# Performance work log

Hardware: AMD Instinct MI355X
Metric: run time of the kernel (lower is better)

The kernel has to match this reference:

```python
import jax, jax.numpy as jnp
import numpy as np

N_NODES = 20000
N_EDGES = 320000
IN_DIM = 128
HID = 256
HEADS = 8
DH = HID // HEADS  # 32
LAYERS = 3
NUM_GRAPHS = 64
OUT_DIM = 10
SLOPE = 0.2  # DGL GATv2Conv default negative_slope


def setup_inputs() -> dict:
    key = jax.random.key(0)
    ks = jax.random.split(key, 20)
    s_in = 1.0 / np.sqrt(IN_DIM)
    s_h = 1.0 / np.sqrt(HID)
    s_h2 = 1.0 / np.sqrt(HID // 2)
    return {
        "feature": jax.random.normal(ks[0], (N_NODES, IN_DIM), jnp.float32),
        "W_in": jax.random.normal(ks[1], (IN_DIM, HID), jnp.float32) * s_in,
        "b_in": jax.random.normal(ks[2], (HID,), jnp.float32) * 0.01,
        "W_src": jax.random.normal(ks[3], (LAYERS, HID, HID), jnp.float32) * s_h,
        "b_src": jax.random.normal(ks[4], (LAYERS, HID), jnp.float32) * 0.01,
        "W_dst": jax.random.normal(ks[5], (LAYERS, HID, HID), jnp.float32) * s_h,
        "b_dst": jax.random.normal(ks[6], (LAYERS, HID), jnp.float32) * 0.01,
        "attn": jax.random.normal(ks[7], (LAYERS, HEADS, DH), jnp.float32) * (1.0 / np.sqrt(DH)),
        "Wc1": jax.random.normal(ks[8], (HID, HID), jnp.float32) * s_h,
        "bc1": jax.random.normal(ks[9], (HID,), jnp.float32) * 0.01,
        "Wc2": jax.random.normal(ks[10], (HID, HID // 2), jnp.float32) * s_h,
        "bc2": jax.random.normal(ks[11], (HID // 2,), jnp.float32) * 0.01,
        "Wc3": jax.random.normal(ks[12], (HID // 2, OUT_DIM), jnp.float32) * s_h2,
        "bc3": jax.random.normal(ks[13], (OUT_DIM,), jnp.float32) * 0.01,
        "src": jax.random.randint(ks[14], (N_EDGES,), 0, N_NODES, jnp.int32),
        "dst": jax.random.randint(ks[15], (N_EDGES,), 0, N_NODES, jnp.int32),
        "graph_ids": jnp.sort(jax.random.randint(ks[16], (N_NODES,), 0, NUM_GRAPHS, jnp.int32)),
    }


def _gatv2_layer(h, Ws, bs, Wd, bd, a, src, dst):
    # DGL GATv2Conv: e_ij = a^T LeakyReLU(W_src h_j + W_dst h_i), edge softmax over
    # incoming edges of dst, scatter-sum of alpha * W_src h_src; residual = Identity
    # (in_feats == heads*out_feats); activation relu.
    n = h.shape[0]
    fs = (h @ Ws + bs).reshape(n, HEADS, DH)  # [N,H,D]
    fd = (h @ Wd + bd).reshape(n, HEADS, DH)
    e = jax.nn.leaky_relu(fs[src] + fd[dst], SLOPE)          # [E,H,D]
    score = jnp.einsum("ehd,hd->eh", e, a)                   # [E,H]
    m = jax.ops.segment_max(score, dst, num_segments=n)       # stable softmax max
    ex = jnp.exp(score - m[dst])
    denom = jax.ops.segment_sum(ex, dst, num_segments=n)
    alpha = ex / denom[dst]                                    # [E,H]
    rst = jax.ops.segment_sum(alpha[:, :, None] * fs[src], dst, num_segments=n)
    out = jax.nn.relu(rst + h.reshape(n, HEADS, DH))          # residual + activation
    return out.reshape(n, HID)


def reference(feature, W_in, b_in, W_src, b_src, W_dst, b_dst, attn,
              Wc1, bc1, Wc2, bc2, Wc3, bc3, src, dst, graph_ids):
    h = feature @ W_in + b_in
    for l in range(LAYERS):
        h = _gatv2_layer(h, W_src[l], b_src[l], W_dst[l], b_dst[l], attn[l], src, dst)
    # dgl.sum_nodes over batched graph -> per-graph segment sum
    hg = jax.ops.segment_sum(h, graph_ids, num_segments=NUM_GRAPHS)  # [G,HID]
    # classifier (dropout is identity in eval mode)
    x = jax.nn.relu(hg @ Wc1 + bc1)
    x = jax.nn.relu(x @ Wc2 + bc2)
    return x @ Wc3 + bc3  # [G,OUT_DIM]
```

## Files before the change

### kernel.cpp

```cpp
#include <hip/hip_runtime.h>
#include <hip/hip_bf16.h>
#include <math.h>

#define N_NODES 20000
#define N_EDGES 320000
#define IN_DIM 128
#define HID 256
#define HEADS 8
#define DH 32
#define LAYERS 3
#define NUM_GRAPHS 64
#define OUT_DIM 10
#define SLOPE 0.2f

#define NBKT 5
#define N_BINS (N_NODES * NBKT)
#define SCAN_BLK 1024
#define SCAN_NBLK ((N_BINS + SCAN_BLK - 1) / SCAN_BLK)

typedef __bf16 bf16x8 __attribute__((ext_vector_type(8)));
typedef float f32x4 __attribute__((ext_vector_type(4)));

static __device__ __forceinline__ unsigned short f2bfbits(float v) {
    __bf16 b = (__bf16)v;
    return __builtin_bit_cast(unsigned short, b);
}
static __device__ __forceinline__ void unpack8(uint4 u, float* f) {
    unsigned p0 = u.x, p1 = u.y, p2 = u.z, p3 = u.w;
    f[0] = __builtin_bit_cast(float, p0 << 16);
    f[1] = __builtin_bit_cast(float, p0 & 0xffff0000u);
    f[2] = __builtin_bit_cast(float, p1 << 16);
    f[3] = __builtin_bit_cast(float, p1 & 0xffff0000u);
    f[4] = __builtin_bit_cast(float, p2 << 16);
    f[5] = __builtin_bit_cast(float, p2 & 0xffff0000u);
    f[6] = __builtin_bit_cast(float, p3 << 16);
    f[7] = __builtin_bit_cast(float, p3 & 0xffff0000u);
}
static __device__ __forceinline__ void unpack4(uint2 u, float* f) {
    f[0] = __builtin_bit_cast(float, u.x << 16);
    f[1] = __builtin_bit_cast(float, u.x & 0xffff0000u);
    f[2] = __builtin_bit_cast(float, u.y << 16);
    f[3] = __builtin_bit_cast(float, u.y & 0xffff0000u);
}

typedef const __attribute__((address_space(1))) unsigned int* as1_u32p;
typedef __attribute__((address_space(3))) unsigned int* as3_u32p;
static __device__ __forceinline__ void async_cp16(const unsigned short* g, unsigned short* l) {
    __builtin_amdgcn_global_load_lds((as1_u32p)g, (as3_u32p)l, 16, 0, 0);
}

#define CAST_N4 (N_NODES * IN_DIM / 4)
#define WTRANS_TOTAL (IN_DIM * HID + 6 * HID * HID)
#define ZERO_TOTAL (N_BINS + NUM_GRAPHS * HID)
#define PREP_TOTAL (CAST_N4 + WTRANS_TOTAL + ZERO_TOTAL)
__global__ void prep_kernel(const float* __restrict__ feat,
                            const float* __restrict__ Win,
                            const float* __restrict__ Wsrc,
                            const float* __restrict__ Wdst,
                            unsigned short* __restrict__ featH,
                            unsigned short* __restrict__ WinT,
                            unsigned short* __restrict__ WT,
                            int* __restrict__ cnt, float* __restrict__ hg) {
    int idx = blockIdx.x * blockDim.x + threadIdx.x;
    if (idx < CAST_N4) {
        float4 v = ((const float4*)feat)[idx];
        ushort4 o;
        o.x = f2bfbits(v.x); o.y = f2bfbits(v.y);
        o.z = f2bfbits(v.z); o.w = f2bfbits(v.w);
        ((ushort4*)featH)[idx] = o;
    } else if (idx < CAST_N4 + WTRANS_TOTAL) {
        int j = idx - CAST_N4;
        if (j < IN_DIM * HID) {
            int n = j / IN_DIM, k = j % IN_DIM;
            WinT[j] = f2bfbits(Win[k * HID + n]);
        } else {
            int r6 = j - IN_DIM * HID;
            int mat = r6 >> 16;
            int r = r6 & 65535;
            int n = r >> 8, k = r & 255;
            const float* base = (mat < 3) ? (Wsrc + (size_t)mat * 65536)
                                          : (Wdst + (size_t)(mat - 3) * 65536);
            WT[r6] = f2bfbits(base[k * 256 + n]);
        }
    } else if (idx < PREP_TOTAL) {
        int z = idx - CAST_N4 - WTRANS_TOTAL;
        if (z < N_BINS) cnt[z] = 0;
        else hg[z - N_BINS] = 0.f;
    }
}

__global__ void count_kernel(const int* __restrict__ src, const int* __restrict__ dst,
                             int* __restrict__ cnt) {
    int e = blockIdx.x * blockDim.x + threadIdx.x;
    if (e < N_EDGES) atomicAdd(&cnt[dst[e] * NBKT + (src[e] >> 12)], 1);
}

__global__ __launch_bounds__(1024) void scan_partial(const int* __restrict__ cnt,
                                                     int* __restrict__ bsum) {
    __shared__ int wsum[16];
    int t = threadIdx.x;
    int idx = blockIdx.x * SCAN_BLK + t;
    int x = (idx < N_BINS) ? cnt[idx] : 0;
    int v = x;
#pragma unroll
    for (int d = 1; d < 64; d <<= 1) v += __shfl_xor(v, d, 64);
    if ((t & 63) == 0) wsum[t >> 6] = v;
    __syncthreads();
    if (t == 0) {
        int s = 0;
#pragma unroll
        for (int i = 0; i < 16; ++i) s += wsum[i];
        bsum[blockIdx.x] = s;
    }
}

__global__ __launch_bounds__(1024) void scan_scatter(const int* __restrict__ cnt,
                                                     const int* __restrict__ bsum,
                                                     int* __restrict__ offs,
                                                     int* __restrict__ cursor) {
    __shared__ int wsum[16];
    __shared__ int bpart[128];
    __shared__ int sbase;
    int t = threadIdx.x;
    int blk = blockIdx.x;
    if (t < 128) bpart[t] = (t < blk) ? bsum[t] : 0;
    __syncthreads();
    if (t < 64) {
        int r = bpart[t] + bpart[t + 64];
#pragma unroll
        for (int d = 1; d < 64; d <<= 1) r += __shfl_xor(r, d, 64);
        if (t == 0) sbase = r;
    }
    int idx = blk * SCAN_BLK + t;
    int x = (idx < N_BINS) ? cnt[idx] : 0;
    int v = x;
#pragma unroll
    for (int d = 1; d < 64; d <<= 1) {
        int u = __shfl_up(v, d, 64);
        if ((t & 63) >= d) v += u;
    }
    if ((t & 63) == 63) wsum[t >> 6] = v;
    __syncthreads();
    if (t < 16) {
        int wv = wsum[t];
#pragma unroll
        for (int d = 1; d < 16; d <<= 1) {
            int u = __shfl_up(wv, d, 64);
            if (t >= d) wv += u;
        }
        wsum[t] = wv;
    }
    __syncthreads();
    int waveoff = (t >> 6) ? wsum[(t >> 6) - 1] : 0;
    int ex = sbase + waveoff + v - x;
    if (idx < N_BINS) { offs[idx] = ex; cursor[idx] = ex; }
    if (blk == SCAN_NBLK - 1 && t == SCAN_BLK - 1) offs[N_BINS] = ex + x;
}

__global__ void fill_kernel(const int* __restrict__ src, const int* __restrict__ dst,
                            int* __restrict__ cursor, int* __restrict__ csr_src) {
    int e = blockIdx.x * blockDim.x + threadIdx.x;
    if (e < N_EDGES) {
        int sv = src[e];
        int p = atomicAdd(&cursor[dst[e] * NBKT + (sv >> 12)], 1);
        csr_src[p] = sv;
    }
}

template <int DUAL>
__global__ __launch_bounds__(256, 4) void mfma_gemm(
    const unsigned short* __restrict__ Ah,
    const unsigned short* __restrict__ BT1, const float* __restrict__ bias1,
    unsigned short* __restrict__ O1,
    const unsigned short* __restrict__ BT2, const float* __restrict__ bias2,
    unsigned short* __restrict__ O2,
    int M, int K, int N) {
    __shared__ __align__(16) unsigned short As[2][64 * 32];
    __shared__ __align__(16) unsigned short Bs1[2][128 * 32];
    __shared__ __align__(16) unsigned short Bs2[DUAL ? 2 : 1][DUAL ? 128 * 32 : 8];

    const int t = threadIdx.x;
    const int wv = t >> 6, lane = t & 63, quad = lane >> 4, l15 = lane & 15;
    const int m0 = blockIdx.x * 64, n0 = blockIdx.y * 128;

    const int sA = wv * 64 + lane;
    const int rA = sA >> 2, cA = (sA & 3) ^ ((rA >> 1) & 3);
    int gmA = m0 + rA; if (gmA >= M) gmA = M - 1;
    const size_t offA = (size_t)gmA * K + cA * 8;
    const int sB0 = wv * 64 + lane, sB1v = sB0 + 256;
    const int rB0 = sB0 >> 2, cB0 = (sB0 & 3) ^ ((rB0 >> 1) & 3);
    const int rB1 = sB1v >> 2, cB1 = (sB1v & 3) ^ ((rB1 >> 1) & 3);
    const size_t offB0 = (size_t)(n0 + rB0) * K + cB0 * 8;
    const size_t offB1 = (size_t)(n0 + rB1) * K + cB1 * 8;

    auto issue = [&](int buf, int k0) {
        async_cp16(Ah + offA + k0, &As[buf][wv * 512]);
        async_cp16(BT1 + offB0 + k0, &Bs1[buf][wv * 512]);
        async_cp16(BT1 + offB1 + k0, &Bs1[buf][2048 + wv * 512]);
        if (DUAL) {
            async_cp16(BT2 + offB0 + k0, &Bs2[buf][wv * 512]);
            async_cp16(BT2 + offB1 + k0, &Bs2[buf][2048 + wv * 512]);
        }
    };

    const int mrow0 = (wv >> 1) * 32;
    const int ncb = (wv & 1) * 64;

    f32x4 zero = {0.f, 0.f, 0.f, 0.f};
    f32x4 acc1[2][4], acc2[2][4];
#pragma unroll
    for (int mi = 0; mi < 2; ++mi)
#pragma unroll
        for (int t4 = 0; t4 < 4; ++t4) { acc1[mi][t4] = zero; acc2[mi][t4] = zero; }

    issue(0, 0);
    int buf = 0;
    for (int k0 = 0; k0 < K; k0 += 32, buf ^= 1) {
        __syncthreads();
        if (k0 + 32 < K) issue(buf ^ 1, k0 + 32);

        bf16x8 aF[2];
#pragma unroll
        for (int mi = 0; mi < 2; ++mi) {
            int row = mrow0 + mi * 16 + l15;
            int aoff = row * 32 + ((quad ^ ((row >> 1) & 3)) << 3);
            aF[mi] = __builtin_bit_cast(bf16x8, *(const uint4*)(&As[buf][0] + aoff));
        }
#pragma unroll
        for (int t4 = 0; t4 < 4; ++t4) {
            int brow = ncb + t4 * 16 + l15;
            int boff = brow * 32 + ((quad ^ ((brow >> 1) & 3)) << 3);
            bf16x8 b1 = __builtin_bit_cast(bf16x8, *(const uint4*)(&Bs1[buf][0] + boff));
#pragma unroll
            for (int mi = 0; mi < 2; ++mi)
                acc1[mi][t4] = __builtin_amdgcn_mfma_f32_16x16x32_bf16(aF[mi], b1, acc1[mi][t4], 0, 0, 0);
            if (DUAL) {
                bf16x8 b2 = __builtin_bit_cast(bf16x8, *(const uint4*)(&Bs2[buf][0] + boff));
#pragma unroll
                for (int mi = 0; mi < 2; ++mi)
                    acc2[mi][t4] = __builtin_amdgcn_mfma_f32_16x16x32_bf16(aF[mi], b2, acc2[mi][t4], 0, 0, 0);
            }
        }
    }

    float bia1[4], bia2[4];
#pragma unroll
    for (int t4 = 0; t4 < 4; ++t4) {
        bia1[t4] = bias1[n0 + ncb + t4 * 16 + l15];
        bia2[t4] = DUAL ? bias2[n0 + ncb + t4 * 16 + l15] : 0.f;
    }
#pragma unroll
    for (int mi = 0; mi < 2; ++mi) {
#pragma unroll
        for (int t4 = 0; t4 < 4; ++t4) {
            int gn = n0 + ncb + t4 * 16 + l15;
#pragma unroll
            for (int r = 0; r < 4; ++r) {
                int gm = m0 + mrow0 + mi * 16 + quad * 4 + r;
                if (gm < M) {
                    float v = acc1[mi][t4][r] + bia1[t4];
                    O1[(size_t)gm * N + gn] = f2bfbits(v);
                    if (DUAL) {
                        float v2 = acc2[mi][t4][r] + bia2[t4];
                        O2[(size_t)gm * N + gn] = f2bfbits(v2);
                    }
                }
            }
        }
    }
}

__global__ __launch_bounds__(256) void gat_agg2(
    const unsigned short* __restrict__ fsb, const unsigned short* __restrict__ fdb,
    unsigned short* __restrict__ hb, const int* __restrict__ offs,
    const int* __restrict__ csr_src, const float* __restrict__ attn_l) {
    int tid = threadIdx.x;
    int node = (blockIdx.x * blockDim.x + tid) >> 5;
    if (node >= N_NODES) return;
    int l32 = tid & 31;
    int dbase = l32 * 8;
    int abase = (l32 >> 2) * DH + (l32 & 3) * 8;

    float a[8];
#pragma unroll
    for (int j = 0; j < 8; ++j) a[j] = attn_l[abase + j];

    float fdv[8];
    unpack8(*(const uint4*)(fdb + (size_t)node * HID + dbase), fdv);

    float ssum0 = 0.f, ssum1 = 0.f;
    float acc0[8], acc1[8];
#pragma unroll
    for (int j = 0; j < 8; ++j) { acc0[j] = 0.f; acc1[j] = 0.f; }

    auto procE = [&](uint4 u, float* acc, float& ssum) {
        float fsv[8];
        unpack8(u, fsv);
        float p = 0.f;
#pragma unroll
        for (int j = 0; j < 8; ++j) {
            float e = fsv[j] + fdv[j];
            e = fmaxf(e, SLOPE * e);
            p += e * a[j];
        }
        p += __shfl_xor(p, 1, 64);
        p += __shfl_xor(p, 2, 64);
        float w = __expf(p);
        ssum += w;
#pragma unroll
        for (int j = 0; j < 8; ++j) acc[j] += w * fsv[j];
    };

    const unsigned short* fsl = fsb + dbase;
    int beg = offs[node * NBKT], end = offs[node * NBKT + NBKT];
    int nfull = (end - beg) >> 2;
    const int limit = beg + nfull * 4;

    uint4 cu0, cu1, cu2, cu3;
    int ci0, ci1, ci2, ci3;
    int base = beg + 8;
    bool have = (nfull >= 1);
    bool haveN = (nfull >= 2);
    if (have) {
        int s0 = csr_src[beg], s1 = csr_src[beg + 1];
        int s2 = csr_src[beg + 2], s3 = csr_src[beg + 3];
        if (haveN) {
            ci0 = csr_src[beg + 4]; ci1 = csr_src[beg + 5];
            ci2 = csr_src[beg + 6]; ci3 = csr_src[beg + 7];
        }
        cu0 = *(const uint4*)(fsl + (size_t)s0 * HID);
        cu1 = *(const uint4*)(fsl + (size_t)s1 * HID);
        cu2 = *(const uint4*)(fsl + (size_t)s2 * HID);
        cu3 = *(const uint4*)(fsl + (size_t)s3 * HID);
    }
    while (have) {
        uint4 nu0, nu1, nu2, nu3;
        int ni0, ni1, ni2, ni3;
        if (haveN) {
            nu0 = *(const uint4*)(fsl + (size_t)ci0 * HID);
            nu1 = *(const uint4*)(fsl + (size_t)ci1 * HID);
            nu2 = *(const uint4*)(fsl + (size_t)ci2 * HID);
            nu3 = *(const uint4*)(fsl + (size_t)ci3 * HID);
        }
        bool haveNN = (base + 4 <= limit);
        if (haveNN) {
            ni0 = csr_src[base]; ni1 = csr_src[base + 1];
            ni2 = csr_src[base + 2]; ni3 = csr_src[base + 3];
        }
        base += 4;
        procE(cu0, acc0, ssum0);
        procE(cu1, acc1, ssum1);
        procE(cu2, acc0, ssum0);
        procE(cu3, acc1, ssum1);
        if (haveN) { cu0 = nu0; cu1 = nu1; cu2 = nu2; cu3 = nu3; }
        if (haveNN) { ci0 = ni0; ci1 = ni1; ci2 = ni2; ci3 = ni3; }
        have = haveN; haveN = haveNN;
    }
    for (int idx = limit; idx < end; ++idx) {
        int sv = csr_src[idx];
        procE(*(const uint4*)(fsl + (size_t)sv * HID), acc0, ssum0);
    }

    float ssum = ssum0 + ssum1;
    float acc[8];
#pragma unroll
    for (int j = 0; j < 8; ++j) acc[j] = acc0[j] + acc1[j];

    float inv = ssum > 0.f ? 1.f / ssum : 0.f;
    float hv[8];
    unpack8(*(const uint4*)(hb + (size_t)node * HID + dbase), hv);
    unsigned short ob[8];
#pragma unroll
    for (int j = 0; j < 8; ++j) {
        float o = fmaxf(acc[j] * inv + hv[j], 0.f);
        ob[j] = f2bfbits(o);
    }
    *(uint4*)(hb + (size_t)node * HID + dbase) = *(uint4*)ob;
}

#define POOL_CHUNK 32
__global__ __launch_bounds__(64) void pool_kernel(const unsigned short* __restrict__ hb,
                                                  const int* __restrict__ gid,
                                                  float* __restrict__ hg) {
    int t = threadIdx.x;
    int n0 = blockIdx.x * POOL_CHUNK;
    int n1 = n0 + POOL_CHUNK; if (n1 > N_NODES) n1 = N_NODES;
    if (n0 >= N_NODES) return;
    float acc[4] = {0.f, 0.f, 0.f, 0.f};
    int cur = gid[n0];
    for (int n = n0; n < n1; ++n) {
        int g = gid[n];
        if (g != cur) {
            atomicAdd(&hg[(size_t)cur * HID + t * 4 + 0], acc[0]);
            atomicAdd(&hg[(size_t)cur * HID + t * 4 + 1], acc[1]);
            atomicAdd(&hg[(size_t)cur * HID + t * 4 + 2], acc[2]);
            atomicAdd(&hg[(size_t)cur * HID + t * 4 + 3], acc[3]);
            acc[0] = acc[1] = acc[2] = acc[3] = 0.f;
            cur = g;
        }
        float v[4];
        unpack4(*(const uint2*)(hb + (size_t)n * HID + t * 4), v);
        acc[0] += v[0]; acc[1] += v[1]; acc[2] += v[2]; acc[3] += v[3];
    }
    atomicAdd(&hg[(size_t)cur * HID + t * 4 + 0], acc[0]);
    atomicAdd(&hg[(size_t)cur * HID + t * 4 + 1], acc[1]);
    atomicAdd(&hg[(size_t)cur * HID + t * 4 + 2], acc[2]);
    atomicAdd(&hg[(size_t)cur * HID + t * 4 + 3], acc[3]);
}

__global__ __launch_bounds__(256) void classifier_kernel(
    const float* __restrict__ hg,
    const float* __restrict__ Wc1, const float* __restrict__ bc1,
    const float* __restrict__ Wc2, const float* __restrict__ bc2,
    const float* __restrict__ Wc3, const float* __restrict__ bc3,
    float* __restrict__ out) {
    __shared__ float xin[HID];
    __shared__ float x1[HID];
    __shared__ float x2[HID / 2];
    int g = blockIdx.x, t = threadIdx.x;
    xin[t] = hg[(size_t)g * HID + t];
    __syncthreads();
    {
        float acc = bc1[t];
        for (int k = 0; k < HID; ++k) acc += xin[k] * Wc1[k * HID + t];
        x1[t] = fmaxf(acc, 0.f);
    }
    __syncthreads();
    if (t < HID / 2) {
        float acc = bc2[t];
        for (int k = 0; k < HID; ++k) acc += x1[k] * Wc2[k * (HID / 2) + t];
        x2[t] = fmaxf(acc, 0.f);
    }
    __syncthreads();
    if (t < OUT_DIM) {
        float acc = bc3[t];
        for (int k = 0; k < HID / 2; ++k) acc += x2[k] * Wc3[k * OUT_DIM + t];
        out[g * OUT_DIM + t] = acc;
    }
}

extern "C" void kernel_launch(void* const* d_in, const int* in_sizes, int n_in,
                              void* d_out, int out_size, void* d_ws, size_t ws_size,
                              hipStream_t stream) {
    const float* feature = (const float*)d_in[0];
    const float* W_in   = (const float*)d_in[1];
    const float* b_in   = (const float*)d_in[2];
    const float* W_src  = (const float*)d_in[3];
    const float* b_src  = (const float*)d_in[4];
    const float* W_dst  = (const float*)d_in[5];
    const float* b_dst  = (const float*)d_in[6];
    const float* attn   = (const float*)d_in[7];
    const float* Wc1    = (const float*)d_in[8];
    const float* bc1    = (const float*)d_in[9];
    const float* Wc2    = (const float*)d_in[10];
    const float* bc2    = (const float*)d_in[11];
    const float* Wc3    = (const float*)d_in[12];
    const float* bc3    = (const float*)d_in[13];
    const int* src     = (const int*)d_in[14];
    const int* dst     = (const int*)d_in[15];
    const int* gid     = (const int*)d_in[16];
    float* out = (float*)d_out;

    char* w = (char*)d_ws;
    auto alloc = [&](size_t bytes) -> void* {
        void* p = (void*)w;
        w += (bytes + 255) & ~(size_t)255;
        return p;
    };
    unsigned short* hb  = (unsigned short*)alloc((size_t)N_NODES * HID * 2);
    unsigned short* fsb = (unsigned short*)alloc((size_t)N_NODES * HID * 2);
    unsigned short* fdb = (unsigned short*)alloc((size_t)N_NODES * HID * 2);
    float* hg    = (float*)alloc((size_t)NUM_GRAPHS * HID * 4);
    int* cnt     = (int*)alloc((size_t)N_BINS * 4);
    int* offs    = (int*)alloc((size_t)(N_BINS + 1) * 4);
    int* cursor  = (int*)alloc((size_t)N_BINS * 4);
    int* csr_src = (int*)alloc((size_t)N_EDGES * 4);
    int* bsum    = (int*)alloc((size_t)SCAN_NBLK * 4);
    unsigned short* WinT = (unsigned short*)alloc((size_t)IN_DIM * HID * 2);
    unsigned short* WT   = (unsigned short*)alloc((size_t)6 * HID * HID * 2);
    unsigned short* featH = (unsigned short*)alloc((size_t)N_NODES * IN_DIM * 2);
    (void)alloc(4096);

    hipLaunchKernelGGL(prep_kernel, dim3((PREP_TOTAL + 255) / 256), dim3(256), 0, stream,
                       feature, W_in, W_src, W_dst, featH, WinT, WT, cnt, hg);

    hipLaunchKernelGGL(count_kernel, dim3((N_EDGES + 255) / 256), dim3(256), 0, stream,
                       src, dst, cnt);
    hipLaunchKernelGGL(scan_partial, dim3(SCAN_NBLK), dim3(SCAN_BLK), 0, stream, cnt, bsum);
    hipLaunchKernelGGL(scan_scatter, dim3(SCAN_NBLK), dim3(SCAN_BLK), 0, stream,
                       cnt, bsum, offs, cursor);
    hipLaunchKernelGGL(fill_kernel, dim3((N_EDGES + 255) / 256), dim3(256), 0, stream,
                       src, dst, cursor, csr_src);

    dim3 ggrid((N_NODES + 63) / 64, HID / 128);

    hipLaunchKernelGGL((mfma_gemm<0>), ggrid, dim3(256), 0, stream,
                       featH, WinT, b_in, hb,
                       (const unsigned short*)nullptr, (const float*)nullptr,
                       (unsigned short*)nullptr,
                       N_NODES, IN_DIM, HID);

    for (int l = 0; l < LAYERS; ++l) {
        hipLaunchKernelGGL((mfma_gemm<1>), ggrid, dim3(256), 0, stream,
                           hb,
                           WT + (size_t)l * HID * HID, b_src + (size_t)l * HID, fsb,
                           WT + (size_t)(3 + l) * HID * HID, b_dst + (size_t)l * HID, fdb,
                           N_NODES, HID, HID);
        hipLaunchKernelGGL(gat_agg2, dim3(N_NODES / 8), dim3(256), 0, stream,
                           fsb, fdb, hb, offs, csr_src, attn + (size_t)l * HEADS * DH);
    }

    hipLaunchKernelGGL(pool_kernel, dim3((N_NODES + POOL_CHUNK - 1) / POOL_CHUNK), dim3(64), 0, stream,
                       hb, gid, hg);
    hipLaunchKernelGGL(classifier_kernel, dim3(NUM_GRAPHS), dim3(256), 0, stream,
                       hg, Wc1, bc1, Wc2, bc2, Wc3, bc3, out);
}
```

Baseline: 313.7 us.

## Fuse preprocessing, CSR build, and pooling into co-scheduled combined kernels

Edge counting now shares a launch with the weight and feature casts. A single-block vectorised scan runs alongside the input GEMM tiles, and the CSR fill runs alongside the first layer's dual GEMM. Graph pooling moves into the classifier kernel: each block binary-searches the sorted graph ids and sums its node range directly, replacing the atomic pool kernel and the zeroing of its buffer. The aim is fewer kernel launches and less serialization, at the cost of a long sequential single-block scan and uneven blocks within the fused grids.

New measurement: 388.2 us. 1.24x slower.

```diff
diff --git a/kernel.cpp b/kernel.cpp
--- a/kernel.cpp
+++ b/kernel.cpp
@@ -15,8 +15,11 @@
 
 #define NBKT 5
 #define N_BINS (N_NODES * NBKT)
-#define SCAN_BLK 1024
-#define SCAN_NBLK ((N_BINS + SCAN_BLK - 1) / SCAN_BLK)
+#define N_BINS4 (N_BINS / 4)
+#define SCAN_CHUNKS ((N_BINS4 + 255) / 256)
+
+#define GEMM_TILES 626
+#define COUNT_BLOCKS 1250
 
 typedef __bf16 bf16x8 __attribute__((ext_vector_type(8)));
 typedef float f32x4 __attribute__((ext_vector_type(4)));
@@ -24,6 +27,9 @@
 static __device__ __forceinline__ unsigned short f2bfbits(float v) {
     __bf16 b = (__bf16)v;
     return __builtin_bit_cast(unsigned short, b);
+}
+static __device__ __forceinline__ float bfu2f(unsigned short v) {
+    return __builtin_bit_cast(float, ((unsigned)v) << 16);
 }
 static __device__ __forceinline__ void unpack8(uint4 u, float* f) {
     unsigned p0 = u.x, p1 = u.y, p2 = u.z, p3 = u.w;
@@ -36,12 +42,6 @@
     f[6] = __builtin_bit_cast(float, p3 << 16);
     f[7] = __builtin_bit_cast(float, p3 & 0xffff0000u);
 }
-static __device__ __forceinline__ void unpack4(uint2 u, float* f) {
-    f[0] = __builtin_bit_cast(float, u.x << 16);
-    f[1] = __builtin_bit_cast(float, u.x & 0xffff0000u);
-    f[2] = __builtin_bit_cast(float, u.y << 16);
-    f[3] = __builtin_bit_cast(float, u.y & 0xffff0000u);
-}
 
 typedef const __attribute__((address_space(1))) unsigned int* as1_u32p;
 typedef __attribute__((address_space(3))) unsigned int* as3_u32p;
@@ -51,24 +51,24 @@
 
 #define CAST_N4 (N_NODES * IN_DIM / 4)
 #define WTRANS_TOTAL (IN_DIM * HID + 6 * HID * HID)
-#define ZERO_TOTAL (N_BINS + NUM_GRAPHS * HID)
-#define PREP_TOTAL (CAST_N4 + WTRANS_TOTAL + ZERO_TOTAL)
-__global__ void prep_kernel(const float* __restrict__ feat,
-                            const float* __restrict__ Win,
-                            const float* __restrict__ Wsrc,
-                            const float* __restrict__ Wdst,
-                            unsigned short* __restrict__ featH,
-                            unsigned short* __restrict__ WinT,
-                            unsigned short* __restrict__ WT,
-                            int* __restrict__ cnt, float* __restrict__ hg) {
-    int idx = blockIdx.x * blockDim.x + threadIdx.x;
+#define PREP_TOTAL (CAST_N4 + WTRANS_TOTAL)
+#define PREP_BLOCKS (PREP_TOTAL / 256)
+
+static __device__ void prep_item(int idx,
+                                 const float* __restrict__ feat,
+                                 const float* __restrict__ Win,
+                                 const float* __restrict__ Wsrc,
+                                 const float* __restrict__ Wdst,
+                                 unsigned short* __restrict__ featH,
+                                 unsigned short* __restrict__ WinT,
+                                 unsigned short* __restrict__ WT) {
     if (idx < CAST_N4) {
         float4 v = ((const float4*)feat)[idx];
         ushort4 o;
         o.x = f2bfbits(v.x); o.y = f2bfbits(v.y);
         o.z = f2bfbits(v.z); o.w = f2bfbits(v.w);
         ((ushort4*)featH)[idx] = o;
-    } else if (idx < CAST_N4 + WTRANS_TOTAL) {
+    } else {
         int j = idx - CAST_N4;
         if (j < IN_DIM * HID) {
             int n = j / IN_DIM, k = j % IN_DIM;
@@ -82,106 +82,59 @@
                                           : (Wdst + (size_t)(mat - 3) * 65536);
             WT[r6] = f2bfbits(base[k * 256 + n]);
         }
-    } else if (idx < PREP_TOTAL) {
-        int z = idx - CAST_N4 - WTRANS_TOTAL;
-        if (z < N_BINS) cnt[z] = 0;
-        else hg[z - N_BINS] = 0.f;
-    }
-}
-
-__global__ void count_kernel(const int* __restrict__ src, const int* __restrict__ dst,
-                             int* __restrict__ cnt) {
-    int e = blockIdx.x * blockDim.x + threadIdx.x;
-    if (e < N_EDGES) atomicAdd(&cnt[dst[e] * NBKT + (src[e] >> 12)], 1);
-}
-
-__global__ __launch_bounds__(1024) void scan_partial(const int* __restrict__ cnt,
-                                                     int* __restrict__ bsum) {
-    __shared__ int wsum[16];
-    int t = threadIdx.x;
-    int idx = blockIdx.x * SCAN_BLK + t;
-    int x = (idx < N_BINS) ? cnt[idx] : 0;
-    int v = x;
-#pragma unroll
-    for (int d = 1; d < 64; d <<= 1) v += __shfl_xor(v, d, 64);
-    if ((t & 63) == 0) wsum[t >> 6] = v;
-    __syncthreads();
-    if (t == 0) {
-        int s = 0;
-#pragma unroll
-        for (int i = 0; i < 16; ++i) s += wsum[i];
-        bsum[blockIdx.x] = s;
-    }
-}
-
-__global__ __launch_bounds__(1024) void scan_scatter(const int* __restrict__ cnt,
-                                                     const int* __restrict__ bsum,
-                                                     int* __restrict__ offs,
-                                                     int* __restrict__ cursor) {
-    __shared__ int wsum[16];
-    __shared__ int bpart[128];
-    __shared__ int sbase;
-    int t = threadIdx.x;
-    int blk = blockIdx.x;
-    if (t < 128) bpart[t] = (t < blk) ? bsum[t] : 0;
-    __syncthreads();
-    if (t < 64) {
-        int r = bpart[t] + bpart[t + 64];
-#pragma unroll
-        for (int d = 1; d < 64; d <<= 1) r += __shfl_xor(r, d, 64);
-        if (t == 0) sbase = r;
-    }
-    int idx = blk * SCAN_BLK + t;
-    int x = (idx < N_BINS) ? cnt[idx] : 0;
-    int v = x;
-#pragma unroll
-    for (int d = 1; d < 64; d <<= 1) {
-        int u = __shfl_up(v, d, 64);
-        if ((t & 63) >= d) v += u;
-    }
-    if ((t & 63) == 63) wsum[t >> 6] = v;
-    __syncthreads();
-    if (t < 16) {
-        int wv = wsum[t];
-#pragma unroll
-        for (int d = 1; d < 16; d <<= 1) {
-            int u = __shfl_up(wv, d, 64);
-            if (t >= d) wv += u;
-        }
-        wsum[t] = wv;
-    }
-    __syncthreads();
-    int waveoff = (t >> 6) ? wsum[(t >> 6) - 1] : 0;
-    int ex = sbase + waveoff + v - x;
-    if (idx < N_BINS) { offs[idx] = ex; cursor[idx] = ex; }
-    if (blk == SCAN_NBLK - 1 && t == SCAN_BLK - 1) offs[N_BINS] = ex + x;
-}
-
-__global__ void fill_kernel(const int* __restrict__ src, const int* __restrict__ dst,
-                            int* __restrict__ cursor, int* __restrict__ csr_src) {
-    int e = blockIdx.x * blockDim.x + threadIdx.x;
-    if (e < N_EDGES) {
-        int sv = src[e];
-        int p = atomicAdd(&cursor[dst[e] * NBKT + (sv >> 12)], 1);
-        csr_src[p] = sv;
-    }
+    }
+}
+
+static __device__ void scan_block(const int* __restrict__ cnt, int* __restrict__ offs,
+                                  int* __restrict__ cursor, int t, int* wsum) {
+    int running = 0;
+    const int4* c4 = (const int4*)cnt;
+    for (int c = 0; c < SCAN_CHUNKS; ++c) {
+        int idx4 = c * 256 + t;
+        int4 x = make_int4(0, 0, 0, 0);
+        if (idx4 < N_BINS4) x = c4[idx4];
+        int tsum = x.x + x.y + x.z + x.w;
+        int v = tsum;
+#pragma unroll
+        for (int d = 1; d < 64; d <<= 1) {
+            int u = __shfl_up(v, d, 64);
+            if ((t & 63) >= d) v += u;
+        }
+        if ((t & 63) == 63) wsum[t >> 6] = v;
+        __syncthreads();
+        int w0 = wsum[0], w1 = wsum[1], w2 = wsum[2], w3 = wsum[3];
+        int wid = t >> 6;
+        int waveoff = 0;
+        if (wid > 0) waveoff += w0;
+        if (wid > 1) waveoff += w1;
+        if (wid > 2) waveoff += w2;
+        int ex = running + waveoff + (v - tsum);
+        if (idx4 < N_BINS4) {
+            int4 o;
+            o.x = ex; o.y = ex + x.x; o.z = o.y + x.y; o.w = o.z + x.z;
+            ((int4*)offs)[idx4] = o;
+            ((int4*)cursor)[idx4] = o;
+        }
+        running += w0 + w1 + w2 + w3;
+        __syncthreads();
+    }
+    if (t == 0) offs[N_BINS] = running;
 }
 
 template <int DUAL>
-__global__ __launch_bounds__(256, 4) void mfma_gemm(
-    const unsigned short* __restrict__ Ah,
-    const unsigned short* __restrict__ BT1, const float* __restrict__ bias1,
-    unsigned short* __restrict__ O1,
-    const unsigned short* __restrict__ BT2, const float* __restrict__ bias2,
-    unsigned short* __restrict__ O2,
-    int M, int K, int N) {
-    __shared__ __align__(16) unsigned short As[2][64 * 32];
-    __shared__ __align__(16) unsigned short Bs1[2][128 * 32];
-    __shared__ __align__(16) unsigned short Bs2[DUAL ? 2 : 1][DUAL ? 128 * 32 : 8];
-
-    const int t = threadIdx.x;
+static __device__ void gemm_tile(int mt, int nt, int t,
+                                 const unsigned short* __restrict__ Ah,
+                                 const unsigned short* __restrict__ BT1,
+                                 const float* __restrict__ bias1,
+                                 unsigned short* __restrict__ O1,
+                                 const unsigned short* __restrict__ BT2,
+                                 const float* __restrict__ bias2,
+                                 unsigned short* __restrict__ O2,
+                                 int M, int K, int N,
+                                 unsigned short* AsP, unsigned short* Bs1P,
+                                 unsigned short* Bs2P) {
     const int wv = t >> 6, lane = t & 63, quad = lane >> 4, l15 = lane & 15;
-    const int m0 = blockIdx.x * 64, n0 = blockIdx.y * 128;
+    const int m0 = mt * 64, n0 = nt * 128;
 
     const int sA = wv * 64 + lane;
     const int rA = sA >> 2, cA = (sA & 3) ^ ((rA >> 1) & 3);
@@ -194,12 +147,12 @@
     const size_t offB1 = (size_t)(n0 + rB1) * K + cB1 * 8;
 
     auto issue = [&](int buf, int k0) {
-        async_cp16(Ah + offA + k0, &As[buf][wv * 512]);
-        async_cp16(BT1 + offB0 + k0, &Bs1[buf][wv * 512]);
-        async_cp16(BT1 + offB1 + k0, &Bs1[buf][2048 + wv * 512]);
+        async_cp16(Ah + offA + k0, AsP + buf * 2048 + wv * 512);
+        async_cp16(BT1 + offB0 + k0, Bs1P + buf * 4096 + wv * 512);
+        async_cp16(BT1 + offB1 + k0, Bs1P + buf * 4096 + 2048 + wv * 512);
         if (DUAL) {
-            async_cp16(BT2 + offB0 + k0, &Bs2[buf][wv * 512]);
-            async_cp16(BT2 + offB1 + k0, &Bs2[buf][2048 + wv * 512]);
+            async_cp16(BT2 + offB0 + k0, Bs2P + buf * 4096 + wv * 512);
+            async_cp16(BT2 + offB1 + k0, Bs2P + buf * 4096 + 2048 + wv * 512);
         }
     };
 
@@ -224,18 +177,18 @@
         for (int mi = 0; mi < 2; ++mi) {
             int row = mrow0 + mi * 16 + l15;
             int aoff = row * 32 + ((quad ^ ((row >> 1) & 3)) << 3);
-            aF[mi] = __builtin_bit_cast(bf16x8, *(const uint4*)(&As[buf][0] + aoff));
+            aF[mi] = __builtin_bit_cast(bf16x8, *(const uint4*)(AsP + buf * 2048 + aoff));
         }
 #pragma unroll
         for (int t4 = 0; t4 < 4; ++t4) {
             int brow = ncb + t4 * 16 + l15;
             int boff = brow * 32 + ((quad ^ ((brow >> 1) & 3)) << 3);
-            bf16x8 b1 = __builtin_bit_cast(bf16x8, *(const uint4*)(&Bs1[buf][0] + boff));
+            bf16x8 b1 = __builtin_bit_cast(bf16x8, *(const uint4*)(Bs1P + buf * 4096 + boff));
 #pragma unroll
             for (int mi = 0; mi < 2; ++mi)
                 acc1[mi][t4] = __builtin_amdgcn_mfma_f32_16x16x32_bf16(aF[mi], b1, acc1[mi][t4], 0, 0, 0);
             if (DUAL) {
-                bf16x8 b2 = __builtin_bit_cast(bf16x8, *(const uint4*)(&Bs2[buf][0] + boff));
+                bf16x8 b2 = __builtin_bit_cast(bf16x8, *(const uint4*)(Bs2P + buf * 4096 + boff));
 #pragma unroll
                 for (int mi = 0; mi < 2; ++mi)
                     acc2[mi][t4] = __builtin_amdgcn_mfma_f32_16x16x32_bf16(aF[mi], b2, acc2[mi][t4], 0, 0, 0);
@@ -270,14 +223,16 @@
     }
 }
 
-__global__ __launch_bounds__(256) void gat_agg2(
-    const unsigned short* __restrict__ fsb, const unsigned short* __restrict__ fdb,
-    unsigned short* __restrict__ hb, const int* __restrict__ offs,
-    const int* __restrict__ csr_src, const float* __restrict__ attn_l) {
-    int tid = threadIdx.x;
-    int node = (blockIdx.x * blockDim.x + tid) >> 5;
+static __device__ void agg_unit(int u, int t,
+                                const unsigned short* __restrict__ fsb,
+                                const unsigned short* __restrict__ fdb,
+                                unsigned short* __restrict__ hb,
+                                const int* __restrict__ offs,
+                                const int* __restrict__ csr_src,
+                                const float* __restrict__ attn_l) {
+    int node = u * 8 + (t >> 5);
     if (node >= N_NODES) return;
-    int l32 = tid & 31;
+    int l32 = t & 31;
     int dbase = l32 * 8;
     int abase = (l32 >> 2) * DH + (l32 & 3) * 8;
 
@@ -293,9 +248,9 @@
 #pragma unroll
     for (int j = 0; j < 8; ++j) { acc0[j] = 0.f; acc1[j] = 0.f; }
 
-    auto procE = [&](uint4 u, float* acc, float& ssum) {
+    auto procE = [&](uint4 uu, float* acc, float& ssum) {
         float fsv[8];
-        unpack8(u, fsv);
+        unpack8(uu, fsv);
         float p = 0.f;
 #pragma unroll
         for (int j = 0; j < 8; ++j) {
@@ -378,38 +333,86 @@
     *(uint4*)(hb + (size_t)node * HID + dbase) = *(uint4*)ob;
 }
 
-#define POOL_CHUNK 32
-__global__ __launch_bounds__(64) void pool_kernel(const unsigned short* __restrict__ hb,
-                                                  const int* __restrict__ gid,
-                                                  float* __restrict__ hg) {
-    int t = threadIdx.x;
-    int n0 = blockIdx.x * POOL_CHUNK;
-    int n1 = n0 + POOL_CHUNK; if (n1 > N_NODES) n1 = N_NODES;
-    if (n0 >= N_NODES) return;
-    float acc[4] = {0.f, 0.f, 0.f, 0.f};
-    int cur = gid[n0];
-    for (int n = n0; n < n1; ++n) {
-        int g = gid[n];
-        if (g != cur) {
-            atomicAdd(&hg[(size_t)cur * HID + t * 4 + 0], acc[0]);
-            atomicAdd(&hg[(size_t)cur * HID + t * 4 + 1], acc[1]);
-            atomicAdd(&hg[(size_t)cur * HID + t * 4 + 2], acc[2]);
-            atomicAdd(&hg[(size_t)cur * HID + t * 4 + 3], acc[3]);
-            acc[0] = acc[1] = acc[2] = acc[3] = 0.f;
-            cur = g;
-        }
-        float v[4];
-        unpack4(*(const uint2*)(hb + (size_t)n * HID + t * 4), v);
-        acc[0] += v[0]; acc[1] += v[1]; acc[2] += v[2]; acc[3] += v[3];
-    }
-    atomicAdd(&hg[(size_t)cur * HID + t * 4 + 0], acc[0]);
-    atomicAdd(&hg[(size_t)cur * HID + t * 4 + 1], acc[1]);
-    atomicAdd(&hg[(size_t)cur * HID + t * 4 + 2], acc[2]);
-    atomicAdd(&hg[(size_t)cur * HID + t * 4 + 3], acc[3]);
-}
-
-__global__ __launch_bounds__(256) void classifier_kernel(
-    const float* __restrict__ hg,
+__global__ void prep_count_kernel(const float* __restrict__ feat,
+                                  const float* __restrict__ Win,
+                                  const float* __restrict__ Wsrc,
+                                  const float* __restrict__ Wdst,
+                                  unsigned short* __restrict__ featH,
+                                  unsigned short* __restrict__ WinT,
+                                  unsigned short* __restrict__ WT,
+                                  const int* __restrict__ src,
+                                  const int* __restrict__ dst,
+                                  int* __restrict__ cnt) {
+    int bid = blockIdx.x;
+    if (bid < PREP_BLOCKS) {
+        prep_item(bid * 256 + threadIdx.x, feat, Win, Wsrc, Wdst, featH, WinT, WT);
+    } else {
+        int e = (bid - PREP_BLOCKS) * 256 + threadIdx.x;
+        if (e < N_EDGES) atomicAdd(&cnt[dst[e] * NBKT + (src[e] >> 12)], 1);
+    }
+}
+
+__global__ __launch_bounds__(256, 4) void gemm0_scan_kernel(
+    const unsigned short* __restrict__ featH, const unsigned short* __restrict__ WinT,
+    const float* __restrict__ b_in, unsigned short* __restrict__ hb,
+    const int* __restrict__ cnt, int* __restrict__ offs, int* __restrict__ cursor) {
+    __shared__ __align__(16) unsigned short smem[20480];
+    int bid = blockIdx.x;
+    if (bid < GEMM_TILES) {
+        gemm_tile<0>(bid >> 1, bid & 1, threadIdx.x, featH, WinT, b_in, hb,
+                     (const unsigned short*)nullptr, (const float*)nullptr,
+                     (unsigned short*)nullptr, N_NODES, IN_DIM, HID,
+                     smem, smem + 4096, smem + 12288);
+    } else {
+        scan_block(cnt, offs, cursor, threadIdx.x, (int*)(void*)smem);
+    }
+}
+
+__global__ __launch_bounds__(256, 4) void gemm1_fill_kernel(
+    const unsigned short* __restrict__ hb,
+    const unsigned short* __restrict__ WTs, const float* __restrict__ bs,
+    unsigned short* __restrict__ fsb,
+    const unsigned short* __restrict__ WTd, const float* __restrict__ bd,
+    unsigned short* __restrict__ fdb,
+    const int* __restrict__ src, const int* __restrict__ dst,
+    int* __restrict__ cursor, int* __restrict__ csr_src) {
+    __shared__ __align__(16) unsigned short smem[20480];
+    int bid = blockIdx.x;
+    if (bid < GEMM_TILES) {
+        gemm_tile<1>(bid >> 1, bid & 1, threadIdx.x, hb, WTs, bs, fsb, WTd, bd, fdb,
+                     N_NODES, HID, HID, smem, smem + 4096, smem + 12288);
+    } else {
+        int e = (bid - GEMM_TILES) * 256 + threadIdx.x;
+        if (e < N_EDGES) {
+            int sv = src[e];
+            int p = atomicAdd(&cursor[dst[e] * NBKT + (sv >> 12)], 1);
+            csr_src[p] = sv;
+        }
+    }
+}
+
+__global__ __launch_bounds__(256, 4) void gemm_kernel(
+    const unsigned short* __restrict__ Ah,
+    const unsigned short* __restrict__ BT1, const float* __restrict__ bias1,
+    unsigned short* __restrict__ O1,
+    const unsigned short* __restrict__ BT2, const float* __restrict__ bias2,
+    unsigned short* __restrict__ O2) {
+    __shared__ __align__(16) unsigned short smem[20480];
+    gemm_tile<1>(blockIdx.x, blockIdx.y, threadIdx.x, Ah, BT1, bias1, O1,
+                 BT2, bias2, O2, N_NODES, HID, HID, smem, smem + 4096, smem + 12288);
+}
+
+__global__ __launch_bounds__(256) void agg_kernel(const unsigned short* __restrict__ fsb,
+                                                  const unsigned short* __restrict__ fdb,
+                                                  unsigned short* __restrict__ hb,
+                                                  const int* __restrict__ offs,
+                                                  const int* __restrict__ csr_src,
+                                                  const float* __restrict__ attn_l) {
+    agg_unit(blockIdx.x, threadIdx.x, fsb, fdb, hb, offs, csr_src, attn_l);
+}
+
+__global__ __launch_bounds__(256) void poolcls_kernel(
+    const unsigned short* __restrict__ hb, const int* __restrict__ gid,
     const float* __restrict__ Wc1, const float* __restrict__ bc1,
     const float* __restrict__ Wc2, const float* __restrict__ bc2,
     const float* __restrict__ Wc3, const float* __restrict__ bc3,
@@ -418,8 +421,26 @@
     __shared__ float x1[HID];
     __shared__ float x2[HID / 2];
     int g = blockIdx.x, t = threadIdx.x;
-    xin[t] = hg[(size_t)g * HID + t];
+
+    int lo = 0, hi = N_NODES;
+    while (lo < hi) { int mid = (lo + hi) >> 1; if (gid[mid] < g) lo = mid + 1; else hi = mid; }
+    int s0 = lo;
+    hi = N_NODES;
+    while (lo < hi) { int mid = (lo + hi) >> 1; if (gid[mid] < g + 1) lo = mid + 1; else hi = mid; }
+    int e0 = lo;
+
+    float a0 = 0.f, a1 = 0.f, a2 = 0.f, a3 = 0.f;
+    int n = s0;
+    for (; n + 4 <= e0; n += 4) {
+        a0 += bfu2f(hb[(size_t)(n + 0) * HID + t]);
+        a1 += bfu2f(hb[(size_t)(n + 1) * HID + t]);
+        a2 += bfu2f(hb[(size_t)(n + 2) * HID + t]);
+        a3 += bfu2f(hb[(size_t)(n + 3) * HID + t]);
+    }
+    for (; n < e0; ++n) a0 += bfu2f(hb[(size_t)n * HID + t]);
+    xin[t] = (a0 + a1) + (a2 + a3);
     __syncthreads();
+
     {
         float acc = bc1[t];
         for (int k = 0; k < HID; ++k) acc += xin[k] * Wc1[k * HID + t];
@@ -470,48 +491,37 @@
     unsigned short* hb  = (unsigned short*)alloc((size_t)N_NODES * HID * 2);
     unsigned short* fsb = (unsigned short*)alloc((size_t)N_NODES * HID * 2);
     unsigned short* fdb = (unsigned short*)alloc((size_t)N_NODES * HID * 2);
-    float* hg    = (float*)alloc((size_t)NUM_GRAPHS * HID * 4);
     int* cnt     = (int*)alloc((size_t)N_BINS * 4);
-    int* offs    = (int*)alloc((size_t)(N_BINS + 1) * 4);
+    int* offs    = (int*)alloc((size_t)(N_BINS + 4) * 4);
     int* cursor  = (int*)alloc((size_t)N_BINS * 4);
     int* csr_src = (int*)alloc((size_t)N_EDGES * 4);
-    int* bsum    = (int*)alloc((size_t)SCAN_NBLK * 4);
     unsigned short* WinT = (unsigned short*)alloc((size_t)IN_DIM * HID * 2);
     unsigned short* WT   = (unsigned short*)alloc((size_t)6 * HID * HID * 2);
     unsigned short* featH = (unsigned short*)alloc((size_t)N_NODES * IN_DIM * 2);
     (void)alloc(4096);
 
-    hipLaunchKernelGGL(prep_kernel, dim3((PREP_TOTAL + 255) / 256), dim3(256), 0, stream,
-                       feature, W_in, W_src, W_dst, featH, WinT, WT, cnt, hg);
-
-    hipLaunchKernelGGL(count_kernel, dim3((N_EDGES + 255) / 256), dim3(256), 0, stream,
-                       src, dst, cnt);
-    hipLaunchKernelGGL(scan_partial, dim3(SCAN_NBLK), dim3(SCAN_BLK), 0, stream, cnt, bsum);
-    hipLaunchKernelGGL(scan_scatter, dim3(SCAN_NBLK), dim3(SCAN_BLK), 0, stream,
-                       cnt, bsum, offs, cursor);
-    hipLaunchKernelGGL(fill_kernel, dim3((N_EDGES + 255) / 256), dim3(256), 0, stream,
+    hipMemsetAsync(cnt, 0, (size_t)N_BINS * 4, stream);
+
+    hipLaunchKernelGGL(prep_count_kernel, dim3(PREP_BLOCKS + COUNT_BLOCKS), dim3(256), 0, stream,
+                       feature, W_in, W_src, W_dst, featH, WinT, WT, src, dst, cnt);
+
+    hipLaunchKernelGGL(gemm0_scan_kernel, dim3(GEMM_TILES + 1), dim3(256), 0, stream,
+                       featH, WinT, b_in, hb, cnt, offs, cursor);
+
+    hipLaunchKernelGGL(gemm1_fill_kernel, dim3(GEMM_TILES + COUNT_BLOCKS), dim3(256), 0, stream,
+                       hb, WT, b_src, fsb, WT + 3 * 65536, b_dst, fdb,
                        src, dst, cursor, csr_src);
 
-    dim3 ggrid((N_NODES + 63) / 64, HID / 128);
-
-    hipLaunchKernelGGL((mfma_gemm<0>), ggrid, dim3(256), 0, stream,
-                       featH, WinT, b_in, hb,
-                       (const unsigned short*)nullptr, (const float*)nullptr,
-                       (unsigned short*)nullptr,
-                       N_NODES, IN_DIM, HID);
-
     for (int l = 0; l < LAYERS; ++l) {
-        hipLaunchKernelGGL((mfma_gemm<1>), ggrid, dim3(256), 0, stream,
-                           hb,
-                           WT + (size_t)l * HID * HID, b_src + (size_t)l * HID, fsb,
-                           WT + (size_t)(3 + l) * HID * HID, b_dst + (size_t)l * HID, fdb,
-                           N_NODES, HID, HID);
-        hipLaunchKernelGGL(gat_agg2, dim3(N_NODES / 8), dim3(256), 0, stream,
+        hipLaunchKernelGGL(agg_kernel, dim3(N_NODES / 8), dim3(256), 0, stream,
                            fsb, fdb, hb, offs, csr_src, attn + (size_t)l * HEADS * DH);
-    }
-
-    hipLaunchKernelGGL(pool_kernel, dim3((N_NODES + POOL_CHUNK - 1) / POOL_CHUNK), dim3(64), 0, stream,
-                       hb, gid, hg);
-    hipLaunchKernelGGL(classifier_kernel, dim3(NUM_GRAPHS), dim3(256), 0, stream,
-                       hg, Wc1, bc1, Wc2, bc2, Wc3, bc3, out);
-}
+        if (l + 1 < LAYERS) {
+            hipLaunchKernelGGL(gemm_kernel, dim3(313, 2), dim3(256), 0, stream,
+                               hb, WT + (size_t)(l + 1) * 65536, b_src + (size_t)(l + 1) * HID, fsb,
+                               WT + (size_t)(4 + l) * 65536, b_dst + (size_t)(l + 1) * HID, fdb);
+        }
+    }
+
+    hipLaunchKernelGGL(poolcls_kernel, dim3(NUM_GRAPHS), dim3(256), 0, stream,
+                       hb, gid, Wc1, bc1, Wc2, bc2, Wc3, bc3, out);
+}
```
